# Optimization experiments

Hardware: AMD Instinct MI355X
Metric: run time of the kernel (lower is better)

## Reference

```python
import jax, jax.numpy as jnp
import numpy as np

B, SQ, SE, D, H, DFF = 16, 512, 512, 512, 8, 2048
DH = D // H
EPS = 1e-6


def _ln(x, g, b):
    mu = jnp.mean(x, axis=-1, keepdims=True)
    var = jnp.mean((x - mu) ** 2, axis=-1, keepdims=True)
    return (x - mu) * jax.lax.rsqrt(var + EPS) * g + b


def _mha(v, k, q, mask, wq_w, wq_b, wk_w, wk_b, wv_w, wv_b, do_w, do_b):
    b = q.shape[0]
    def split(t):  # [b, s, D] -> [b, H, s, DH]
        return t.reshape(b, -1, H, DH).transpose(0, 2, 1, 3)
    qh = split(q @ wq_w + wq_b)
    kh = split(k @ wk_w + wk_b)
    vh = split(v @ wv_w + wv_b)
    logits = jnp.einsum('bhqd,bhkd->bhqk', qh, kh) / jnp.sqrt(jnp.float32(DH))
    logits = logits + mask * (-1e9)
    attn = jax.nn.softmax(logits, axis=-1)
    out = jnp.einsum('bhqk,bhkd->bhqd', attn, vh)
    out = out.transpose(0, 2, 1, 3).reshape(b, -1, D)
    # output projection has GELU activation (exact erf, keras default)
    out = jax.nn.gelu(out @ do_w + do_b, approximate=False)
    return out, attn


def setup_inputs() -> dict:
    key = jax.random.key(0)
    ks = jax.random.split(key, 32)
    s = 0.02  # weight scale
    inp = {
        'x': jax.random.normal(ks[0], (B, SQ, D), dtype=jnp.float32),
        'enc_fc': jax.random.normal(ks[1], (B, SE, D), dtype=jnp.float32),
        'enc_ff': jax.random.normal(ks[2], (B, SE, D), dtype=jnp.float32),
        # causal look-ahead mask: 1 where attention is disallowed
        'look_ahead_mask': jnp.triu(jnp.ones((SQ, SQ), jnp.float32), k=1)[None, None],
        # random padding mask over encoder positions (1 = masked)
        'padding_mask': (jax.random.uniform(ks[3], (B, 1, 1, SE)) < 0.1).astype(jnp.float32),
    }
    i = 4
    for p in ('m1', 'm2'):
        for w in ('wq', 'wk', 'wv', 'do'):
            inp[f'{p}_{w}_w'] = jax.random.normal(ks[i], (D, D), dtype=jnp.float32) * s; i += 1
            inp[f'{p}_{w}_b'] = jnp.zeros((D,), jnp.float32)
    inp['ffn_w1'] = jax.random.normal(ks[i], (D, DFF), dtype=jnp.float32) * s; i += 1
    inp['ffn_b1'] = jnp.zeros((DFF,), jnp.float32)
    inp['ffn_w2'] = jax.random.normal(ks[i], (DFF, D), dtype=jnp.float32) * s; i += 1
    inp['ffn_b2'] = jnp.zeros((D,), jnp.float32)
    for ln in ('ln1', 'ln2', 'ln3'):
        inp[f'{ln}_g'] = jnp.ones((D,), jnp.float32)
        inp[f'{ln}_b'] = jnp.zeros((D,), jnp.float32)
    return inp


def reference(x, enc_fc, enc_ff, look_ahead_mask, padding_mask,
              m1_wq_w, m1_wq_b, m1_wk_w, m1_wk_b, m1_wv_w, m1_wv_b, m1_do_w, m1_do_b,
              m2_wq_w, m2_wq_b, m2_wk_w, m2_wk_b, m2_wv_w, m2_wv_b, m2_do_w, m2_do_b,
              ffn_w1, ffn_b1, ffn_w2, ffn_b2,
              ln1_g, ln1_b, ln2_g, ln2_b, ln3_g, ln3_b):
    # self-attention (v=k=q=x), causal mask
    attn1, aw1 = _mha(x, x, x, look_ahead_mask,
                      m1_wq_w, m1_wq_b, m1_wk_w, m1_wk_b, m1_wv_w, m1_wv_b, m1_do_w, m1_do_b)
    out1 = _ln(attn1 + x, ln1_g, ln1_b)  # dropout identity in eval
    # cross-attention: v=enc_ff, k=enc_fc, q=out1, padding mask
    attn2, aw2 = _mha(enc_ff, enc_fc, out1, padding_mask,
                      m2_wq_w, m2_wq_b, m2_wk_w, m2_wk_b, m2_wv_w, m2_wv_b, m2_do_w, m2_do_b)
    out2 = _ln(attn2 + out1, ln2_g, ln2_b)
    # FFN: relu dense -> (dropout identity) -> dense
    ff = jax.nn.relu(out2 @ ffn_w1 + ffn_b1) @ ffn_w2 + ffn_b2
    out3 = _ln(ff + out2, ln3_g, ln3_b)
    return out3, aw1, aw2
```

## Files before the change

kernel.cpp:

```cpp
#include <hip/hip_runtime.h>
#include <stdint.h>
#include <math.h>

typedef unsigned short u16;
typedef __attribute__((ext_vector_type(8))) __bf16 bf16x8;
typedef __attribute__((ext_vector_type(4))) float f32x4;

#define NB 16
#define NSQ 512
#define NSE 512
#define ND 512
#define NH 8
#define NDH 64
#define NDFF 2048

__device__ __forceinline__ u16 f2b(float f) {
  uint32_t u = __float_as_uint(f);
  u = (u + 0x7FFFu + ((u >> 16) & 1u)) >> 16;
  return (u16)u;
}
__device__ __forceinline__ float b2f(uint32_t h) {
  return __uint_as_float(h << 16);
}

__device__ __forceinline__ void gl_lds16(const u16* g, u16* l) {
  __builtin_amdgcn_global_load_lds(
      (const __attribute__((address_space(1))) void*)g,
      (__attribute__((address_space(3))) void*)l, 16, 0, 0);
}

template <int NBX>
__device__ __forceinline__ int swz8(int bx) {
  return (bx & 7) * (NBX / 8) + (bx >> 3);
}

struct Prep {
  const float *x, *fc, *ff;
  u16 *xb, *fcb, *ffb;
  const float* w8[8];
  u16* o8[8];
  const float *w1, *w2;
  u16 *w1t, *w2t;
};

__device__ __forceinline__ void tr32(const float* __restrict__ W,
                                     u16* __restrict__ Wt, int K, int N, int bx,
                                     int by, float (*t)[33]) {
  const int tid = threadIdx.x, tx = tid & 31, ty = tid >> 5;
  const int n0 = bx * 32, k0 = by * 32;
#pragma unroll
  for (int i = 0; i < 32; i += 8)
    t[ty + i][tx] = W[(size_t)(k0 + ty + i) * N + n0 + tx];
  __syncthreads();
#pragma unroll
  for (int i = 0; i < 32; i += 8)
    Wt[(size_t)(n0 + ty + i) * K + k0 + tx] = f2b(t[tx][ty + i]);
}

__global__ void k_prep(Prep p) {
  __shared__ float t[32][33];
  const int blk = blockIdx.x;
  if (blk < 6144) {
    const int plane = blk >> 11;
    const float* src = plane == 0 ? p.x : (plane == 1 ? p.fc : p.ff);
    u16* dst = plane == 0 ? p.xb : (plane == 1 ? p.fcb : p.ffb);
    const int i = (blk & 2047) * 256 + threadIdx.x;
    const float4* q = (const float4*)(src + (size_t)i * 8);
    float4 v0 = q[0], v1 = q[1];
    uint4 o;
    o.x = (uint32_t)f2b(v0.x) | ((uint32_t)f2b(v0.y) << 16);
    o.y = (uint32_t)f2b(v0.z) | ((uint32_t)f2b(v0.w) << 16);
    o.z = (uint32_t)f2b(v1.x) | ((uint32_t)f2b(v1.y) << 16);
    o.w = (uint32_t)f2b(v1.z) | ((uint32_t)f2b(v1.w) << 16);
    *(uint4*)(dst + (size_t)i * 8) = o;
  } else if (blk < 8192) {
    const int b2 = blk - 6144, z = b2 >> 8, bi = b2 & 255;
    tr32(p.w8[z], p.o8[z], 512, 512, bi & 15, bi >> 4, t);
  } else if (blk < 9216) {
    const int b2 = blk - 8192;
    tr32(p.w1, p.w1t, 512, 2048, b2 & 63, b2 >> 6, t);
  } else {
    const int b2 = blk - 9216;
    tr32(p.w2, p.w2t, 2048, 512, b2 & 15, b2 >> 4, t);
  }
}

enum { EPI_GELU = 2, EPI_RELU = 3, EPI_NONE = 4 };

template <int BM>
__device__ __forceinline__ void gemm_core(const u16* __restrict__ A,
                                          const u16* __restrict__ Bt, int K,
                                          int brow, int bcol, u16* As, u16* Bs,
                                          f32x4 (&acc)[BM / 32][4]) {
  const int tid = threadIdx.x, lane = tid & 63, wid = tid >> 6;
  const int wr = wid >> 1, wc = wid & 1;
  const int l15 = lane & 15, g4 = lane >> 4;
  const int sc8 = (lane & 7) * 8;
  const int srow = wid * 8 + (lane >> 3);
  const int nt = K >> 6;
  for (int t = 0; t < nt; ++t) {
    const int k0 = t << 6;
    if (t) __syncthreads();
#pragma unroll
    for (int v = 0; v < BM / 32; ++v)
      gl_lds16(A + (size_t)(brow + v * 32 + srow) * K + k0 + sc8,
               As + (v * 32 + wid * 8) * 64);
#pragma unroll
    for (int v = 0; v < 4; ++v)
      gl_lds16(Bt + (size_t)(bcol + v * 32 + srow) * K + k0 + sc8,
               Bs + (v * 32 + wid * 8) * 64);
    __syncthreads();
#pragma unroll
    for (int kk = 0; kk < 2; ++kk) {
      bf16x8 af[BM / 32], bfr[4];
#pragma unroll
      for (int m = 0; m < BM / 32; ++m)
        af[m] = *(const bf16x8*)(As + (wr * (BM / 2) + m * 16 + l15) * 64 +
                                 kk * 32 + g4 * 8);
#pragma unroll
      for (int n = 0; n < 4; ++n)
        bfr[n] = *(const bf16x8*)(Bs + (wc * 64 + n * 16 + l15) * 64 +
                                  kk * 32 + g4 * 8);
#pragma unroll
      for (int m = 0; m < BM / 32; ++m)
#pragma unroll
        for (int n = 0; n < 4; ++n)
          acc[m][n] =
              __builtin_amdgcn_mfma_f32_16x16x32_bf16(af[m], bfr[n], acc[m][n], 0, 0, 0);
    }
  }
}

template <int BM, int NBX, int EPI>
__global__ __launch_bounds__(256, 3) void k_gemm(
    const u16* __restrict__ A, const u16* __restrict__ Bt,
    const float* __restrict__ bias, u16* __restrict__ out, int K, int N) {
  __shared__ u16 As[BM * 64];
  __shared__ u16 Bs[128 * 64];
  f32x4 acc[BM / 32][4] = {};
  const int brow = swz8<NBX>(blockIdx.x) * BM, bcol = blockIdx.y * 128;
  gemm_core<BM>(A, Bt, K, brow, bcol, As, Bs, acc);
  const int lane = threadIdx.x & 63, wid = threadIdx.x >> 6;
  const int wr = wid >> 1, wc = wid & 1, l15 = lane & 15, g4 = lane >> 4;
#pragma unroll
  for (int m = 0; m < BM / 32; ++m) {
    const int r0 = brow + wr * (BM / 2) + m * 16 + g4 * 4;
#pragma unroll
    for (int n = 0; n < 4; ++n) {
      const int col = bcol + wc * 64 + n * 16 + l15;
      const float bv = bias[col];
#pragma unroll
      for (int j = 0; j < 4; ++j) {
        float vv = acc[m][n][j] + bv;
        if (EPI == EPI_GELU) vv = 0.5f * vv * (1.0f + erff(vv * 0.70710678118654752f));
        if (EPI == EPI_RELU) vv = fmaxf(vv, 0.0f);
        out[(size_t)(r0 + j) * N + col] = f2b(vv);
      }
    }
  }
}

struct QKV {
  const u16* A[3];
  const u16* Bt[3];
  const float* bias[3];
  u16* out[3];
};
__global__ __launch_bounds__(256, 3) void k_gemm_qkv(QKV p) {
  const int z = blockIdx.z;
  __shared__ u16 As[128 * 64];
  __shared__ u16 Bs[128 * 64];
  f32x4 acc[4][4] = {};
  const int brow = swz8<64>(blockIdx.x) * 128, bcol = blockIdx.y * 128;
  gemm_core<128>(p.A[z], p.Bt[z], 512, brow, bcol, As, Bs, acc);
  const int lane = threadIdx.x & 63, wid = threadIdx.x >> 6;
  const int wr = wid >> 1, wc = wid & 1, l15 = lane & 15, g4 = lane >> 4;
  const float* bias = p.bias[z];
  u16* out = p.out[z];
#pragma unroll
  for (int m = 0; m < 4; ++m) {
    const int r0 = brow + wr * 64 + m * 16 + g4 * 4;
#pragma unroll
    for (int n = 0; n < 4; ++n) {
      const int col = bcol + wc * 64 + n * 16 + l15;
      const float bv = bias[col];
      const int h = col >> 6, d = col & 63;
#pragma unroll
      for (int j = 0; j < 4; ++j) {
        const int r = r0 + j, b = r >> 9, s = r & 511;
        const float vv = acc[m][n][j] + bv;
        if (z < 2)
          out[((size_t)(b * NH + h) * NSQ + s) * NDH + d] = f2b(vv);
        else
          out[((size_t)(b * NH + h) * NDH + d) * NSE + s] = f2b(vv);
      }
    }
  }
}

template <int CAUSAL>
__global__ __launch_bounds__(512, 4) void k_attn_fused(
    const u16* __restrict__ qh, const u16* __restrict__ kh,
    const u16* __restrict__ vtg, const float* __restrict__ pmask,
    float* __restrict__ aw, u16* __restrict__ ctx) {
  __shared__ u16 Kt[128 * 64];
  __shared__ u16 Vs[64 * 128];
  __shared__ u16 Ps[128 * 128];

  const int bh = blockIdx.y, b = bh >> 3, h = bh & 7;
  const int brow = blockIdx.x * 128;
  const int tid = threadIdx.x, lane = tid & 63, wid = tid >> 6;
  const int l15 = lane & 15, g4 = lane >> 4;
  const u16* Q = qh + (size_t)bh * NSQ * NDH;
  const u16* Kg = kh + (size_t)bh * NSE * NDH;
  const u16* Vg = vtg + (size_t)bh * NDH * NSE;
  float* awp = aw + (size_t)bh * NSQ * NSE;

  const int krow = wid * 8 + (lane >> 3);
  const int ksw = ((lane & 7) ^ (krow & 7)) * 8;
  const int vsw = (l15 ^ ((wid * 4 + g4) & 7)) * 8;

  bf16x8 qf[2];
#pragma unroll
  for (int kk = 0; kk < 2; ++kk)
    qf[kk] = *(const bf16x8*)(Q + (size_t)(brow + wid * 16 + l15) * NDH +
                              kk * 32 + g4 * 8);

  const int ntile = CAUSAL ? blockIdx.x + 1 : 4;

  auto stage_k = [&](int kb) {
#pragma unroll
    for (int v = 0; v < 2; ++v)
      gl_lds16(Kg + (size_t)(kb + v * 64 + krow) * NDH + ksw,
               Kt + (v * 64 + wid * 8) * 64);
  };
  auto stage_v = [&](int kb) {
#pragma unroll
    for (int v = 0; v < 2; ++v) {
      const int d = v * 32 + wid * 4 + g4;
      gl_lds16(Vg + (size_t)d * NSE + kb + vsw, Vs + (v * 32 + wid * 4) * 128);
    }
  };
  auto computeS = [&](int kb, f32x4(&acc)[8]) {
#pragma unroll
    for (int kk = 0; kk < 2; ++kk) {
      bf16x8 kf[8];
#pragma unroll
      for (int n = 0; n < 8; ++n) {
        const int kr = n * 16 + l15;
        kf[n] = *(const bf16x8*)(Kt + kr * 64 + ((kk * 32 + g4 * 8) ^ ((kr & 7) << 3)));
      }
#pragma unroll
      for (int n = 0; n < 8; ++n)
        acc[n] = __builtin_amdgcn_mfma_f32_16x16x32_bf16(qf[kk], kf[n], acc[n], 0, 0, 0);
    }
    if (!CAUSAL) {
      float pm[8];
#pragma unroll
      for (int n = 0; n < 8; ++n)
        pm[n] = pmask[b * NSE + kb + n * 16 + l15] * (-1e9f);
#pragma unroll
      for (int n = 0; n < 8; ++n)
#pragma unroll
        for (int j = 0; j < 4; ++j)
          acc[n][j] = fminf(acc[n][j] * 0.125f, 60.0f) + pm[n];
    } else {
#pragma unroll
      for (int n = 0; n < 8; ++n) {
        const int key = kb + n * 16 + l15;
#pragma unroll
        for (int j = 0; j < 4; ++j) {
          const int qrow = brow + wid * 16 + g4 * 4 + j;
          acc[n][j] = (key > qrow) ? -1e9f : fminf(acc[n][j] * 0.125f, 60.0f);
        }
      }
    }
  };

  float l4[4] = {0.f, 0.f, 0.f, 0.f};
  for (int t = 0; t < ntile; ++t) {
    if (t) __syncthreads();
    stage_k(t * 128);
    __syncthreads();
    f32x4 acc[8] = {};
    computeS(t * 128, acc);
#pragma unroll
    for (int j = 0; j < 4; ++j) {
      float s = 0.f;
#pragma unroll
      for (int n = 0; n < 8; ++n) s += __expf(acc[n][j]);
#pragma unroll
      for (int o = 1; o < 16; o <<= 1) s += __shfl_xor(s, o, 64);
      l4[j] += s;
    }
  }
  float invl[4];
#pragma unroll
  for (int j = 0; j < 4; ++j) invl[j] = 1.0f / l4[j];

  f32x4 apv[4] = {};
  for (int t = ntile - 1; t >= 0; --t) {
    const int kb = t * 128;
    __syncthreads();
    if (t != ntile - 1) stage_k(kb);
    stage_v(kb);
    __syncthreads();
    f32x4 acc[8] = {};
    computeS(kb, acc);
#pragma unroll
    for (int n = 0; n < 8; ++n) {
      const int col = n * 16 + l15;
#pragma unroll
      for (int j = 0; j < 4; ++j) {
        const int rl = wid * 16 + g4 * 4 + j;
        const float p = __expf(acc[n][j]) * invl[j];
        awp[(size_t)(brow + rl) * NSE + kb + col] = p;
        Ps[rl * 128 + (col ^ ((rl & 7) << 3))] = f2b(p);
      }
    }
#pragma unroll
    for (int kk = 0; kk < 4; ++kk) {
      const int qr = wid * 16 + l15;
      bf16x8 pa =
          *(const bf16x8*)(Ps + qr * 128 + ((kk * 32 + g4 * 8) ^ ((qr & 7) << 3)));
      bf16x8 vb[4];
#pragma unroll
      for (int n = 0; n < 4; ++n) {
        const int d = n * 16 + l15;
        vb[n] = *(const bf16x8*)(Vs + d * 128 + ((kk * 32 + g4 * 8) ^ ((d & 7) << 3)));
      }
#pragma unroll
      for (int n = 0; n < 4; ++n)
        apv[n] = __builtin_amdgcn_mfma_f32_16x16x32_bf16(pa, vb[n], apv[n], 0, 0, 0);
    }
  }

  if (CAUSAL) {
    const float4 z4 = make_float4(0.f, 0.f, 0.f, 0.f);
    for (int t = ntile; t < 4; ++t) {
      const int r = tid >> 2, c0 = t * 128 + (tid & 3) * 32;
      float4* p = (float4*)(awp + (size_t)(brow + r) * NSE + c0);
#pragma unroll
      for (int i = 0; i < 8; ++i) p[i] = z4;
    }
  }

#pragma unroll
  for (int n = 0; n < 4; ++n) {
    const int d = n * 16 + l15;
#pragma unroll
    for (int j = 0; j < 4; ++j) {
      const int r = brow + wid * 16 + g4 * 4 + j;
      ctx[((size_t)(b * NSQ + r)) * ND + h * NDH + d] = f2b(apv[n][j]);
    }
  }
}

template <int B_BF16, int OUT_F32>
__global__ __launch_bounds__(256) void k_res_ln(const u16* __restrict__ a,
                                                const void* __restrict__ bsrc,
                                                const float* __restrict__ g,
                                                const float* __restrict__ bet,
                                                void* __restrict__ outp) {
  const int row = blockIdx.x * 4 + (threadIdx.x >> 6);
  const int lane = threadIdx.x & 63;
  const size_t base = (size_t)row * 512 + lane * 8;
  float s[8];
  {
    uint4 av = *(const uint4*)(a + base);
    s[0] = b2f(av.x & 0xffffu); s[1] = b2f(av.x >> 16);
    s[2] = b2f(av.y & 0xffffu); s[3] = b2f(av.y >> 16);
    s[4] = b2f(av.z & 0xffffu); s[5] = b2f(av.z >> 16);
    s[6] = b2f(av.w & 0xffffu); s[7] = b2f(av.w >> 16);
  }
  if (B_BF16) {
    uint4 bv = *(const uint4*)((const u16*)bsrc + base);
    s[0] += b2f(bv.x & 0xffffu); s[1] += b2f(bv.x >> 16);
    s[2] += b2f(bv.y & 0xffffu); s[3] += b2f(bv.y >> 16);
    s[4] += b2f(bv.z & 0xffffu); s[5] += b2f(bv.z >> 16);
    s[6] += b2f(bv.w & 0xffffu); s[7] += b2f(bv.w >> 16);
  } else {
    const float* bp = (const float*)bsrc + base;
    float4 b0 = *(const float4*)bp, b1 = *(const float4*)(bp + 4);
    s[0] += b0.x; s[1] += b0.y; s[2] += b0.z; s[3] += b0.w;
    s[4] += b1.x; s[5] += b1.y; s[6] += b1.z; s[7] += b1.w;
  }
  float sum = 0.f;
#pragma unroll
  for (int i = 0; i < 8; ++i) sum += s[i];
#pragma unroll
  for (int o = 1; o < 64; o <<= 1) sum += __shfl_xor(sum, o, 64);
  const float mu = sum * (1.0f / 512.0f);
  float vs = 0.f;
#pragma unroll
  for (int i = 0; i < 8; ++i) {
    const float d = s[i] - mu;
    vs += d * d;
  }
#pragma unroll
  for (int o = 1; o < 64; o <<= 1) vs += __shfl_xor(vs, o, 64);
  const float rs = rsqrtf(vs * (1.0f / 512.0f) + 1e-6f);
  float y[8];
#pragma unroll
  for (int i = 0; i < 8; ++i) {
    const int c = lane * 8 + i;
    y[i] = (s[i] - mu) * rs * g[c] + bet[c];
  }
  if (OUT_F32) {
    float* op = (float*)outp + base;
    *(float4*)op = make_float4(y[0], y[1], y[2], y[3]);
    *(float4*)(op + 4) = make_float4(y[4], y[5], y[6], y[7]);
  } else {
    uint4 o;
    o.x = (uint32_t)f2b(y[0]) | ((uint32_t)f2b(y[1]) << 16);
    o.y = (uint32_t)f2b(y[2]) | ((uint32_t)f2b(y[3]) << 16);
    o.z = (uint32_t)f2b(y[4]) | ((uint32_t)f2b(y[5]) << 16);
    o.w = (uint32_t)f2b(y[6]) | ((uint32_t)f2b(y[7]) << 16);
    *(uint4*)((u16*)outp + base) = o;
  }
}

extern "C" void kernel_launch(void* const* d_in, const int* in_sizes, int n_in,
                              void* d_out, int out_size, void* d_ws, size_t ws_size,
                              hipStream_t stream) {
  (void)in_sizes; (void)n_in; (void)out_size; (void)ws_size;
  const float* x = (const float*)d_in[0];
  const float* enc_fc = (const float*)d_in[1];
  const float* enc_ff = (const float*)d_in[2];
  const float* pmask = (const float*)d_in[4];
  const float* w_m1[4] = {(const float*)d_in[5], (const float*)d_in[7],
                          (const float*)d_in[9], (const float*)d_in[11]};
  const float* b_m1[4] = {(const float*)d_in[6], (const float*)d_in[8],
                          (const float*)d_in[10], (const float*)d_in[12]};
  const float* w_m2[4] = {(const float*)d_in[13], (const float*)d_in[15],
                          (const float*)d_in[17], (const float*)d_in[19]};
  const float* b_m2[4] = {(const float*)d_in[14], (const float*)d_in[16],
                          (const float*)d_in[18], (const float*)d_in[20]};
  const float* ffn_w1 = (const float*)d_in[21];
  const float* ffn_b1 = (const float*)d_in[22];
  const float* ffn_w2 = (const float*)d_in[23];
  const float* ffn_b2 = (const float*)d_in[24];
  const float* ln_g[3] = {(const float*)d_in[25], (const float*)d_in[27],
                          (const float*)d_in[29]};
  const float* ln_b[3] = {(const float*)d_in[26], (const float*)d_in[28],
                          (const float*)d_in[30]};

  char* ws = (char*)d_ws;
  const size_t SZB = (size_t)8192 * 512 * 2;
  u16* xb = (u16*)(ws + 0 * SZB);
  u16* fcb = (u16*)(ws + 1 * SZB);
  u16* ffb = (u16*)(ws + 2 * SZB);
  u16* qh = (u16*)(ws + 3 * SZB);
  u16* kh = (u16*)(ws + 4 * SZB);
  u16* vt = (u16*)(ws + 5 * SZB);
  u16* ctx = (u16*)(ws + 6 * SZB);
  u16* ao = (u16*)(ws + 7 * SZB);
  u16* out1 = (u16*)(ws + 8 * SZB);
  u16* out2 = (u16*)(ws + 9 * SZB);
  u16* ffv = (u16*)(ws + 10 * SZB);
  u16* ff1 = (u16*)(ws + 11 * SZB);
  u16* wts = (u16*)(ws + 11 * SZB + (size_t)8192 * 2048 * 2);
  u16 *wt_m1[4], *wt_m2[4];
  for (int i = 0; i < 4; ++i) {
    wt_m1[i] = wts + (size_t)i * 262144;
    wt_m2[i] = wts + (size_t)(4 + i) * 262144;
  }
  u16* w1t = wts + (size_t)8 * 262144;
  u16* w2t = w1t + (size_t)2048 * 512;

  float* out3 = (float*)d_out;
  float* aw1 = out3 + (size_t)NB * NSQ * ND;
  float* aw2 = aw1 + (size_t)NB * NH * NSQ * NSQ;

  Prep pr;
  pr.x = x; pr.fc = enc_fc; pr.ff = enc_ff;
  pr.xb = xb; pr.fcb = fcb; pr.ffb = ffb;
  for (int i = 0; i < 4; ++i) {
    pr.w8[i] = w_m1[i]; pr.o8[i] = wt_m1[i];
    pr.w8[4 + i] = w_m2[i]; pr.o8[4 + i] = wt_m2[i];
  }
  pr.w1 = ffn_w1; pr.w1t = w1t;
  pr.w2 = ffn_w2; pr.w2t = w2t;
  k_prep<<<10240, 256, 0, stream>>>(pr);

  const dim3 gattn(4, 128);
  QKV q1 = {{xb, xb, xb},
            {wt_m1[0], wt_m1[1], wt_m1[2]},
            {b_m1[0], b_m1[1], b_m1[2]},
            {qh, kh, vt}};
  k_gemm_qkv<<<dim3(64, 4, 3), 256, 0, stream>>>(q1);
  k_attn_fused<1><<<gattn, 512, 0, stream>>>(qh, kh, vt, nullptr, aw1, ctx);
  k_gemm<64, 128, EPI_GELU><<<dim3(128, 4), 256, 0, stream>>>(ctx, wt_m1[3], b_m1[3], ao, 512, 512);
  k_res_ln<0, 0><<<2048, 256, 0, stream>>>(ao, x, ln_g[0], ln_b[0], out1);
  QKV q2 = {{out1, fcb, ffb},
            {wt_m2[0], wt_m2[1], wt_m2[2]},
            {b_m2[0], b_m2[1], b_m2[2]},
            {qh, kh, vt}};
  k_gemm_qkv<<<dim3(64, 4, 3), 256, 0, stream>>>(q2);
  k_attn_fused<0><<<gattn, 512, 0, stream>>>(qh, kh, vt, pmask, aw2, ctx);
  k_gemm<64, 128, EPI_GELU><<<dim3(128, 4), 256, 0, stream>>>(ctx, wt_m2[3], b_m2[3], ao, 512, 512);
  k_res_ln<1, 0><<<2048, 256, 0, stream>>>(ao, out1, ln_g[1], ln_b[1], out2);
  k_gemm<128, 64, EPI_RELU><<<dim3(64, 16), 256, 0, stream>>>(out2, w1t, ffn_b1, ff1, 512, 2048);
  k_gemm<64, 128, EPI_NONE><<<dim3(128, 4), 256, 0, stream>>>(ff1, w2t, ffn_b2, ffv, 2048, 512);
  k_res_ln<1, 1><<<2048, 256, 0, stream>>>(ffv, out2, ln_g[2], ln_b[2], (void*)d_out);
}
```

Baseline: 328.4 us.

## Hoist cross-attention K/V projections into first QKV launch and reuse last score tile

The cross-attention K and V projections depend only on encoder inputs, so they move into the first QKV GEMM launch (grid z=5). This fills the grid better and leaves the second launch with only the Q projection. They write into the out2/ffv scratch buffers, which are not used until later. The attention kernel keeps the exponentiated scores of the last tile from pass one, skipping one K restage and score recompute. Attention-weight output is now written as coalesced float4 stores read back from the bf16 Ps tile, which rounds aw1/aw2 to bf16 precision.

Measured after the change: 333.8 us. Within noise of the previous version (+1.7%).

```diff
diff --git a/kernel.cpp b/kernel.cpp
--- a/kernel.cpp
+++ b/kernel.cpp
@@ -161,10 +161,11 @@
 }
 
 struct QKV {
-  const u16* A[3];
-  const u16* Bt[3];
-  const float* bias[3];
-  u16* out[3];
+  const u16* A[5];
+  const u16* Bt[5];
+  const float* bias[5];
+  u16* out[5];
+  int vout[5];
 };
 __global__ __launch_bounds__(256, 3) void k_gemm_qkv(QKV p) {
   const int z = blockIdx.z;
@@ -177,6 +178,7 @@
   const int wr = wid >> 1, wc = wid & 1, l15 = lane & 15, g4 = lane >> 4;
   const float* bias = p.bias[z];
   u16* out = p.out[z];
+  const int vl = p.vout[z];
 #pragma unroll
   for (int m = 0; m < 4; ++m) {
     const int r0 = brow + wr * 64 + m * 16 + g4 * 4;
@@ -189,7 +191,7 @@
       for (int j = 0; j < 4; ++j) {
         const int r = r0 + j, b = r >> 9, s = r & 511;
         const float vv = acc[m][n][j] + bv;
-        if (z < 2)
+        if (vl == 0)
           out[((size_t)(b * NH + h) * NSQ + s) * NDH + d] = f2b(vv);
         else
           out[((size_t)(b * NH + h) * NDH + d) * NSE + s] = f2b(vv);
@@ -278,6 +280,7 @@
   };
 
   float l4[4] = {0.f, 0.f, 0.f, 0.f};
+  f32x4 pcar[8];
   for (int t = 0; t < ntile; ++t) {
     if (t) __syncthreads();
     stage_k(t * 128);
@@ -285,38 +288,47 @@
     f32x4 acc[8] = {};
     computeS(t * 128, acc);
 #pragma unroll
+    for (int n = 0; n < 8; ++n)
+#pragma unroll
+      for (int j = 0; j < 4; ++j) acc[n][j] = __expf(acc[n][j]);
+#pragma unroll
     for (int j = 0; j < 4; ++j) {
       float s = 0.f;
 #pragma unroll
-      for (int n = 0; n < 8; ++n) s += __expf(acc[n][j]);
+      for (int n = 0; n < 8; ++n) s += acc[n][j];
 #pragma unroll
       for (int o = 1; o < 16; o <<= 1) s += __shfl_xor(s, o, 64);
       l4[j] += s;
     }
+    if (t == ntile - 1)
+#pragma unroll
+      for (int n = 0; n < 8; ++n) pcar[n] = acc[n];
   }
   float invl[4];
 #pragma unroll
   for (int j = 0; j < 4; ++j) invl[j] = 1.0f / l4[j];
 
   f32x4 apv[4] = {};
-  for (int t = ntile - 1; t >= 0; --t) {
-    const int kb = t * 128;
-    __syncthreads();
-    if (t != ntile - 1) stage_k(kb);
-    stage_v(kb);
-    __syncthreads();
-    f32x4 acc[8] = {};
-    computeS(kb, acc);
+  auto emitTile = [&](f32x4(&pex)[8], int kb) {
 #pragma unroll
     for (int n = 0; n < 8; ++n) {
       const int col = n * 16 + l15;
 #pragma unroll
       for (int j = 0; j < 4; ++j) {
         const int rl = wid * 16 + g4 * 4 + j;
-        const float p = __expf(acc[n][j]) * invl[j];
-        awp[(size_t)(brow + rl) * NSE + kb + col] = p;
-        Ps[rl * 128 + (col ^ ((rl & 7) << 3))] = f2b(p);
+        Ps[rl * 128 + (col ^ ((rl & 7) << 3))] = f2b(pex[n][j] * invl[j]);
       }
+    }
+#pragma unroll
+    for (int i = 0; i < 4; ++i) {
+      const int rl = wid * 16 + i * 4 + (lane >> 4);
+      const int cb = l15 * 8;
+      uint4 pk = *(const uint4*)(Ps + rl * 128 + (cb ^ ((rl & 7) << 3)));
+      float* dst = awp + (size_t)(brow + rl) * NSE + kb + cb;
+      *(float4*)dst = make_float4(b2f(pk.x & 0xffffu), b2f(pk.x >> 16),
+                                  b2f(pk.y & 0xffffu), b2f(pk.y >> 16));
+      *(float4*)(dst + 4) = make_float4(b2f(pk.z & 0xffffu), b2f(pk.z >> 16),
+                                        b2f(pk.w & 0xffffu), b2f(pk.w >> 16));
     }
 #pragma unroll
     for (int kk = 0; kk < 4; ++kk) {
@@ -333,6 +345,27 @@
       for (int n = 0; n < 4; ++n)
         apv[n] = __builtin_amdgcn_mfma_f32_16x16x32_bf16(pa, vb[n], apv[n], 0, 0, 0);
     }
+  };
+
+  {
+    const int kb = (ntile - 1) * 128;
+    stage_v(kb);
+    __syncthreads();
+    emitTile(pcar, kb);
+  }
+  for (int t = ntile - 2; t >= 0; --t) {
+    const int kb = t * 128;
+    __syncthreads();
+    stage_k(kb);
+    stage_v(kb);
+    __syncthreads();
+    f32x4 acc[8] = {};
+    computeS(kb, acc);
+#pragma unroll
+    for (int n = 0; n < 8; ++n)
+#pragma unroll
+      for (int j = 0; j < 4; ++j) acc[n][j] = __expf(acc[n][j]);
+    emitTile(acc, kb);
   }
 
   if (CAUSAL) {
@@ -468,6 +501,9 @@
   u16* w1t = wts + (size_t)8 * 262144;
   u16* w2t = w1t + (size_t)2048 * 512;
 
+  u16* kh2 = out2;
+  u16* vt2 = ffv;
+
   float* out3 = (float*)d_out;
   float* aw1 = out3 + (size_t)NB * NSQ * ND;
   float* aw2 = aw1 + (size_t)NB * NH * NSQ * NSQ;
@@ -484,20 +520,22 @@
   k_prep<<<10240, 256, 0, stream>>>(pr);
 
   const dim3 gattn(4, 128);
-  QKV q1 = {{xb, xb, xb},
-            {wt_m1[0], wt_m1[1], wt_m1[2]},
-            {b_m1[0], b_m1[1], b_m1[2]},
-            {qh, kh, vt}};
-  k_gemm_qkv<<<dim3(64, 4, 3), 256, 0, stream>>>(q1);
+  QKV q1 = {{xb, xb, xb, fcb, ffb},
+            {wt_m1[0], wt_m1[1], wt_m1[2], wt_m2[1], wt_m2[2]},
+            {b_m1[0], b_m1[1], b_m1[2], b_m2[1], b_m2[2]},
+            {qh, kh, vt, kh2, vt2},
+            {0, 0, 1, 0, 1}};
+  k_gemm_qkv<<<dim3(64, 4, 5), 256, 0, stream>>>(q1);
   k_attn_fused<1><<<gattn, 512, 0, stream>>>(qh, kh, vt, nullptr, aw1, ctx);
   k_gemm<64, 128, EPI_GELU><<<dim3(128, 4), 256, 0, stream>>>(ctx, wt_m1[3], b_m1[3], ao, 512, 512);
   k_res_ln<0, 0><<<2048, 256, 0, stream>>>(ao, x, ln_g[0], ln_b[0], out1);
-  QKV q2 = {{out1, fcb, ffb},
-            {wt_m2[0], wt_m2[1], wt_m2[2]},
-            {b_m2[0], b_m2[1], b_m2[2]},
-            {qh, kh, vt}};
-  k_gemm_qkv<<<dim3(64, 4, 3), 256, 0, stream>>>(q2);
-  k_attn_fused<0><<<gattn, 512, 0, stream>>>(qh, kh, vt, pmask, aw2, ctx);
+  QKV q2 = {{out1, nullptr, nullptr, nullptr, nullptr},
+            {wt_m2[0], nullptr, nullptr, nullptr, nullptr},
+            {b_m2[0], nullptr, nullptr, nullptr, nullptr},
+            {qh, nullptr, nullptr, nullptr, nullptr},
+            {0, 0, 0, 0, 0}};
+  k_gemm_qkv<<<dim3(64, 4, 1), 256, 0, stream>>>(q2);
+  k_attn_fused<0><<<gattn, 512, 0, stream>>>(qh, kh2, vt2, pmask, aw2, ctx);
   k_gemm<64, 128, EPI_GELU><<<dim3(128, 4), 256, 0, stream>>>(ctx, wt_m2[3], b_m2[3], ao, 512, 512);
   k_res_ln<1, 0><<<2048, 256, 0, stream>>>(ao, out1, ln_g[1], ln_b[1], out2);
   k_gemm<128, 64, EPI_RELU><<<dim3(64, 16), 256, 0, stream>>>(out2, w1t, ffn_b1, ff1, 512, 2048);
```

## Double-buffer GEMM LDS tiles and hoist cross-attention K/V projections into first QKV launch

Applied to the files above, without the earlier changes.

The GEMM core now uses double-buffered LDS so the next K-tile's global-to-LDS load is issued while MFMAs run on the current tile. Every GEMM is fixed to a 64x128 tile, and the occupancy hint is raised to 4 blocks per CU. The encoder-side K/V projections for cross-attention depend only on inputs, so they now run in the first QKV launch as extra z-slices, leaving the second launch to compute only Q. Their results are stored in the out2/ffv buffers, which are free until later; this saves one full pass worth of launch and tail overhead but ties correctness to buffer lifetimes.

Result: no change. 334.8 us (+2.0%).

```diff
diff --git a/kernel.cpp b/kernel.cpp
--- a/kernel.cpp
+++ b/kernel.cpp
@@ -87,64 +87,70 @@
 
 enum { EPI_GELU = 2, EPI_RELU = 3, EPI_NONE = 4 };
 
-template <int BM>
-__device__ __forceinline__ void gemm_core(const u16* __restrict__ A,
-                                          const u16* __restrict__ Bt, int K,
-                                          int brow, int bcol, u16* As, u16* Bs,
-                                          f32x4 (&acc)[BM / 32][4]) {
+__device__ __forceinline__ void gemm_core2(const u16* __restrict__ A,
+                                           const u16* __restrict__ Bt, int K,
+                                           int brow, int bcol, u16* As, u16* Bs,
+                                           f32x4 (&acc)[2][4]) {
   const int tid = threadIdx.x, lane = tid & 63, wid = tid >> 6;
   const int wr = wid >> 1, wc = wid & 1;
   const int l15 = lane & 15, g4 = lane >> 4;
   const int sc8 = (lane & 7) * 8;
   const int srow = wid * 8 + (lane >> 3);
   const int nt = K >> 6;
-  for (int t = 0; t < nt; ++t) {
+  const int ASZ = 64 * 64, BSZ = 128 * 64;
+  auto stage = [&](int t, int buf) {
     const int k0 = t << 6;
-    if (t) __syncthreads();
-#pragma unroll
-    for (int v = 0; v < BM / 32; ++v)
+#pragma unroll
+    for (int v = 0; v < 2; ++v)
       gl_lds16(A + (size_t)(brow + v * 32 + srow) * K + k0 + sc8,
-               As + (v * 32 + wid * 8) * 64);
+               As + buf * ASZ + (v * 32 + wid * 8) * 64);
 #pragma unroll
     for (int v = 0; v < 4; ++v)
       gl_lds16(Bt + (size_t)(bcol + v * 32 + srow) * K + k0 + sc8,
-               Bs + (v * 32 + wid * 8) * 64);
-    __syncthreads();
+               Bs + buf * BSZ + (v * 32 + wid * 8) * 64);
+  };
+  stage(0, 0);
+  __syncthreads();
+  int cur = 0;
+  for (int t = 0; t < nt; ++t) {
+    if (t + 1 < nt) stage(t + 1, cur ^ 1);
+    const u16* as = As + cur * ASZ;
+    const u16* bs = Bs + cur * BSZ;
 #pragma unroll
     for (int kk = 0; kk < 2; ++kk) {
-      bf16x8 af[BM / 32], bfr[4];
-#pragma unroll
-      for (int m = 0; m < BM / 32; ++m)
-        af[m] = *(const bf16x8*)(As + (wr * (BM / 2) + m * 16 + l15) * 64 +
-                                 kk * 32 + g4 * 8);
+      bf16x8 af[2], bfr[4];
+#pragma unroll
+      for (int m = 0; m < 2; ++m)
+        af[m] = *(const bf16x8*)(as + (wr * 32 + m * 16 + l15) * 64 + kk * 32 + g4 * 8);
 #pragma unroll
       for (int n = 0; n < 4; ++n)
-        bfr[n] = *(const bf16x8*)(Bs + (wc * 64 + n * 16 + l15) * 64 +
-                                  kk * 32 + g4 * 8);
-#pragma unroll
-      for (int m = 0; m < BM / 32; ++m)
+        bfr[n] = *(const bf16x8*)(bs + (wc * 64 + n * 16 + l15) * 64 + kk * 32 + g4 * 8);
+#pragma unroll
+      for (int m = 0; m < 2; ++m)
 #pragma unroll
         for (int n = 0; n < 4; ++n)
           acc[m][n] =
               __builtin_amdgcn_mfma_f32_16x16x32_bf16(af[m], bfr[n], acc[m][n], 0, 0, 0);
     }
-  }
-}
-
-template <int BM, int NBX, int EPI>
-__global__ __launch_bounds__(256, 3) void k_gemm(
+    __syncthreads();
+    cur ^= 1;
+  }
+}
+
+template <int NBX, int EPI>
+__global__ __launch_bounds__(256, 4) void k_gemm(
     const u16* __restrict__ A, const u16* __restrict__ Bt,
     const float* __restrict__ bias, u16* __restrict__ out, int K, int N) {
-  __shared__ u16 As[BM * 64];
-  __shared__ u16 Bs[128 * 64];
-  f32x4 acc[BM / 32][4] = {};
-  const int brow = swz8<NBX>(blockIdx.x) * BM, bcol = blockIdx.y * 128;
-  gemm_core<BM>(A, Bt, K, brow, bcol, As, Bs, acc);
+  __shared__ u16 As[2 * 64 * 64];
+  __shared__ u16 Bs[2 * 128 * 64];
+  f32x4 acc[2][4] = {};
+  const int brow = swz8<NBX>(blockIdx.x) * 64, bcol = blockIdx.y * 128;
+  gemm_core2(A, Bt, K, brow, bcol, As, Bs, acc);
   const int lane = threadIdx.x & 63, wid = threadIdx.x >> 6;
   const int wr = wid >> 1, wc = wid & 1, l15 = lane & 15, g4 = lane >> 4;
 #pragma unroll
-  for (int m = 0; m < BM / 32; ++m) {
-    const int r0 = brow + wr * (BM / 2) + m * 16 + g4 * 4;
+  for (int m = 0; m < 2; ++m) {
+    const int r0 = brow + wr * 32 + m * 16 + g4 * 4;
 #pragma unroll
     for (int n = 0; n < 4; ++n) {
       const int col = bcol + wc * 64 + n * 16 + l15;
@@ -161,25 +167,27 @@
 }
 
 struct QKV {
-  const u16* A[3];
-  const u16* Bt[3];
-  const float* bias[3];
-  u16* out[3];
+  const u16* A[5];
+  const u16* Bt[5];
+  const float* bias[5];
+  u16* out[5];
+  int vout[5];
 };
-__global__ __launch_bounds__(256, 3) void k_gemm_qkv(QKV p) {
+__global__ __launch_bounds__(256, 4) void k_gemm_qkv(QKV p) {
   const int z = blockIdx.z;
-  __shared__ u16 As[128 * 64];
-  __shared__ u16 Bs[128 * 64];
-  f32x4 acc[4][4] = {};
-  const int brow = swz8<64>(blockIdx.x) * 128, bcol = blockIdx.y * 128;
-  gemm_core<128>(p.A[z], p.Bt[z], 512, brow, bcol, As, Bs, acc);
+  __shared__ u16 As[2 * 64 * 64];
+  __shared__ u16 Bs[2 * 128 * 64];
+  f32x4 acc[2][4] = {};
+  const int brow = swz8<128>(blockIdx.x) * 64, bcol = blockIdx.y * 128;
+  gemm_core2(p.A[z], p.Bt[z], 512, brow, bcol, As, Bs, acc);
   const int lane = threadIdx.x & 63, wid = threadIdx.x >> 6;
   const int wr = wid >> 1, wc = wid & 1, l15 = lane & 15, g4 = lane >> 4;
   const float* bias = p.bias[z];
   u16* out = p.out[z];
-#pragma unroll
-  for (int m = 0; m < 4; ++m) {
-    const int r0 = brow + wr * 64 + m * 16 + g4 * 4;
+  const int vl = p.vout[z];
+#pragma unroll
+  for (int m = 0; m < 2; ++m) {
+    const int r0 = brow + wr * 32 + m * 16 + g4 * 4;
 #pragma unroll
     for (int n = 0; n < 4; ++n) {
       const int col = bcol + wc * 64 + n * 16 + l15;
@@ -189,7 +197,7 @@
       for (int j = 0; j < 4; ++j) {
         const int r = r0 + j, b = r >> 9, s = r & 511;
         const float vv = acc[m][n][j] + bv;
-        if (z < 2)
+        if (vl == 0)
           out[((size_t)(b * NH + h) * NSQ + s) * NDH + d] = f2b(vv);
         else
           out[((size_t)(b * NH + h) * NDH + d) * NSE + s] = f2b(vv);
@@ -468,6 +476,9 @@
   u16* w1t = wts + (size_t)8 * 262144;
   u16* w2t = w1t + (size_t)2048 * 512;
 
+  u16* kh2 = out2;
+  u16* vt2 = ffv;
+
   float* out3 = (float*)d_out;
   float* aw1 = out3 + (size_t)NB * NSQ * ND;
   float* aw2 = aw1 + (size_t)NB * NH * NSQ * NSQ;
@@ -484,23 +495,25 @@
   k_prep<<<10240, 256, 0, stream>>>(pr);
 
   const dim3 gattn(4, 128);
-  QKV q1 = {{xb, xb, xb},
-            {wt_m1[0], wt_m1[1], wt_m1[2]},
-            {b_m1[0], b_m1[1], b_m1[2]},
-            {qh, kh, vt}};
-  k_gemm_qkv<<<dim3(64, 4, 3), 256, 0, stream>>>(q1);
+  QKV q1 = {{xb, xb, xb, fcb, ffb},
+            {wt_m1[0], wt_m1[1], wt_m1[2], wt_m2[1], wt_m2[2]},
+            {b_m1[0], b_m1[1], b_m1[2], b_m2[1], b_m2[2]},
+            {qh, kh, vt, kh2, vt2},
+            {0, 0, 1, 0, 1}};
+  k_gemm_qkv<<<dim3(128, 4, 5), 256, 0, stream>>>(q1);
   k_attn_fused<1><<<gattn, 512, 0, stream>>>(qh, kh, vt, nullptr, aw1, ctx);
-  k_gemm<64, 128, EPI_GELU><<<dim3(128, 4), 256, 0, stream>>>(ctx, wt_m1[3], b_m1[3], ao, 512, 512);
+  k_gemm<128, EPI_GELU><<<dim3(128, 4), 256, 0, stream>>>(ctx, wt_m1[3], b_m1[3], ao, 512, 512);
   k_res_ln<0, 0><<<2048, 256, 0, stream>>>(ao, x, ln_g[0], ln_b[0], out1);
-  QKV q2 = {{out1, fcb, ffb},
-            {wt_m2[0], wt_m2[1], wt_m2[2]},
-            {b_m2[0], b_m2[1], b_m2[2]},
-            {qh, kh, vt}};
-  k_gemm_qkv<<<dim3(64, 4, 3), 256, 0, stream>>>(q2);
-  k_attn_fused<0><<<gattn, 512, 0, stream>>>(qh, kh, vt, pmask, aw2, ctx);
-  k_gemm<64, 128, EPI_GELU><<<dim3(128, 4), 256, 0, stream>>>(ctx, wt_m2[3], b_m2[3], ao, 512, 512);
+  QKV q2 = {{out1, nullptr, nullptr, nullptr, nullptr},
+            {wt_m2[0], nullptr, nullptr, nullptr, nullptr},
+            {b_m2[0], nullptr, nullptr, nullptr, nullptr},
+            {qh, nullptr, nullptr, nullptr, nullptr},
+            {0, 0, 0, 0, 0}};
+  k_gemm_qkv<<<dim3(128, 4, 1), 256, 0, stream>>>(q2);
+  k_attn_fused<0><<<gattn, 512, 0, stream>>>(qh, kh2, vt2, pmask, aw2, ctx);
+  k_gemm<128, EPI_GELU><<<dim3(128, 4), 256, 0, stream>>>(ctx, wt_m2[3], b_m2[3], ao, 512, 512);
   k_res_ln<1, 0><<<2048, 256, 0, stream>>>(ao, out1, ln_g[1], ln_b[1], out2);
-  k_gemm<128, 64, EPI_RELU><<<dim3(64, 16), 256, 0, stream>>>(out2, w1t, ffn_b1, ff1, 512, 2048);
-  k_gemm<64, 128, EPI_NONE><<<dim3(128, 4), 256, 0, stream>>>(ff1, w2t, ffn_b2, ffv, 2048, 512);
+  k_gemm<128, EPI_RELU><<<dim3(128, 16), 256, 0, stream>>>(out2, w1t, ffn_b1, ff1, 512, 2048);
+  k_gemm<128, EPI_NONE><<<dim3(128, 4), 256, 0, stream>>>(ff1, w2t, ffn_b2, ffv, 2048, 512);
   k_res_ln<1, 1><<<2048, 256, 0, stream>>>(ffv, out2, ln_g[2], ln_b[2], (void*)d_out);
 }
```

## Double-buffer K tiles in attention, balance causal block order, use nontemporal stores

Applied to the files above, without the earlier changes.

The attention kernel now double-buffers the K tile in shared memory, so the next tile is prefetched while the current one is computed, and one barrier per iteration is removed. The 1D grid is remapped so causal query blocks are ordered heavy/light in a balanced way: the first half of the grid takes row blocks 0,1 and the second half takes 3,2. Attention-weight stores and the zero fill now use nontemporal stores to avoid polluting the cache. This adds 16KB of shared memory per block, which may lower occupancy.

Result: slower. 352.8 us (+7.4%).

```diff
diff --git a/kernel.cpp b/kernel.cpp
--- a/kernel.cpp
+++ b/kernel.cpp
@@ -203,12 +203,17 @@
     const u16* __restrict__ qh, const u16* __restrict__ kh,
     const u16* __restrict__ vtg, const float* __restrict__ pmask,
     float* __restrict__ aw, u16* __restrict__ ctx) {
-  __shared__ u16 Kt[128 * 64];
+  __shared__ u16 Kt[2][128 * 64];
   __shared__ u16 Vs[64 * 128];
   __shared__ u16 Ps[128 * 128];
 
-  const int bh = blockIdx.y, b = bh >> 3, h = bh & 7;
-  const int brow = blockIdx.x * 128;
+  const int jb = blockIdx.x;
+  const int lo = jb & 255;
+  const int bh = lo & 127;
+  const int sel = lo >> 7;
+  const int bx = (jb >> 8) == 0 ? sel : 3 - sel;
+  const int b = bh >> 3, h = bh & 7;
+  const int brow = bx * 128;
   const int tid = threadIdx.x, lane = tid & 63, wid = tid >> 6;
   const int l15 = lane & 15, g4 = lane >> 4;
   const u16* Q = qh + (size_t)bh * NSQ * NDH;
@@ -226,13 +231,13 @@
     qf[kk] = *(const bf16x8*)(Q + (size_t)(brow + wid * 16 + l15) * NDH +
                               kk * 32 + g4 * 8);
 
-  const int ntile = CAUSAL ? blockIdx.x + 1 : 4;
-
-  auto stage_k = [&](int kb) {
+  const int ntile = CAUSAL ? bx + 1 : 4;
+
+  auto stage_k = [&](int kb, int buf) {
 #pragma unroll
     for (int v = 0; v < 2; ++v)
       gl_lds16(Kg + (size_t)(kb + v * 64 + krow) * NDH + ksw,
-               Kt + (v * 64 + wid * 8) * 64);
+               Kt[buf] + (v * 64 + wid * 8) * 64);
   };
   auto stage_v = [&](int kb) {
 #pragma unroll
@@ -241,14 +246,15 @@
       gl_lds16(Vg + (size_t)d * NSE + kb + vsw, Vs + (v * 32 + wid * 4) * 128);
     }
   };
-  auto computeS = [&](int kb, f32x4(&acc)[8]) {
+  auto computeS = [&](int kb, int buf, f32x4(&acc)[8]) {
+    const u16* kt = Kt[buf];
 #pragma unroll
     for (int kk = 0; kk < 2; ++kk) {
       bf16x8 kf[8];
 #pragma unroll
       for (int n = 0; n < 8; ++n) {
         const int kr = n * 16 + l15;
-        kf[n] = *(const bf16x8*)(Kt + kr * 64 + ((kk * 32 + g4 * 8) ^ ((kr & 7) << 3)));
+        kf[n] = *(const bf16x8*)(kt + kr * 64 + ((kk * 32 + g4 * 8) ^ ((kr & 7) << 3)));
       }
 #pragma unroll
       for (int n = 0; n < 8; ++n)
@@ -278,12 +284,13 @@
   };
 
   float l4[4] = {0.f, 0.f, 0.f, 0.f};
+  stage_k(0, 0);
+  __syncthreads();
   for (int t = 0; t < ntile; ++t) {
-    if (t) __syncthreads();
-    stage_k(t * 128);
-    __syncthreads();
+    const int cur = t & 1;
+    if (t + 1 < ntile) stage_k((t + 1) * 128, cur ^ 1);
     f32x4 acc[8] = {};
-    computeS(t * 128, acc);
+    computeS(t * 128, cur, acc);
 #pragma unroll
     for (int j = 0; j < 4; ++j) {
       float s = 0.f;
@@ -293,6 +300,7 @@
       for (int o = 1; o < 16; o <<= 1) s += __shfl_xor(s, o, 64);
       l4[j] += s;
     }
+    __syncthreads();
   }
   float invl[4];
 #pragma unroll
@@ -301,12 +309,12 @@
   f32x4 apv[4] = {};
   for (int t = ntile - 1; t >= 0; --t) {
     const int kb = t * 128;
+    const int cur = t & 1;
+    if (t > 0) stage_k((t - 1) * 128, cur ^ 1);
+    stage_v(kb);
+    f32x4 acc[8] = {};
+    computeS(kb, cur, acc);
     __syncthreads();
-    if (t != ntile - 1) stage_k(kb);
-    stage_v(kb);
-    __syncthreads();
-    f32x4 acc[8] = {};
-    computeS(kb, acc);
 #pragma unroll
     for (int n = 0; n < 8; ++n) {
       const int col = n * 16 + l15;
@@ -314,7 +322,7 @@
       for (int j = 0; j < 4; ++j) {
         const int rl = wid * 16 + g4 * 4 + j;
         const float p = __expf(acc[n][j]) * invl[j];
-        awp[(size_t)(brow + rl) * NSE + kb + col] = p;
+        __builtin_nontemporal_store(p, awp + (size_t)(brow + rl) * NSE + kb + col);
         Ps[rl * 128 + (col ^ ((rl & 7) << 3))] = f2b(p);
       }
     }
@@ -333,15 +341,16 @@
       for (int n = 0; n < 4; ++n)
         apv[n] = __builtin_amdgcn_mfma_f32_16x16x32_bf16(pa, vb[n], apv[n], 0, 0, 0);
     }
+    __syncthreads();
   }
 
   if (CAUSAL) {
-    const float4 z4 = make_float4(0.f, 0.f, 0.f, 0.f);
+    const f32x4 z4 = {0.f, 0.f, 0.f, 0.f};
     for (int t = ntile; t < 4; ++t) {
       const int r = tid >> 2, c0 = t * 128 + (tid & 3) * 32;
-      float4* p = (float4*)(awp + (size_t)(brow + r) * NSE + c0);
-#pragma unroll
-      for (int i = 0; i < 8; ++i) p[i] = z4;
+      f32x4* p = (f32x4*)(awp + (size_t)(brow + r) * NSE + c0);
+#pragma unroll
+      for (int i = 0; i < 8; ++i) __builtin_nontemporal_store(z4, p + i);
     }
   }
 
@@ -483,13 +492,12 @@
   pr.w2 = ffn_w2; pr.w2t = w2t;
   k_prep<<<10240, 256, 0, stream>>>(pr);
 
-  const dim3 gattn(4, 128);
   QKV q1 = {{xb, xb, xb},
             {wt_m1[0], wt_m1[1], wt_m1[2]},
             {b_m1[0], b_m1[1], b_m1[2]},
             {qh, kh, vt}};
   k_gemm_qkv<<<dim3(64, 4, 3), 256, 0, stream>>>(q1);
-  k_attn_fused<1><<<gattn, 512, 0, stream>>>(qh, kh, vt, nullptr, aw1, ctx);
+  k_attn_fused<1><<<512, 512, 0, stream>>>(qh, kh, vt, nullptr, aw1, ctx);
   k_gemm<64, 128, EPI_GELU><<<dim3(128, 4), 256, 0, stream>>>(ctx, wt_m1[3], b_m1[3], ao, 512, 512);
   k_res_ln<0, 0><<<2048, 256, 0, stream>>>(ao, x, ln_g[0], ln_b[0], out1);
   QKV q2 = {{out1, fcb, ffb},
@@ -497,7 +505,7 @@
             {b_m2[0], b_m2[1], b_m2[2]},
             {qh, kh, vt}};
   k_gemm_qkv<<<dim3(64, 4, 3), 256, 0, stream>>>(q2);
-  k_attn_fused<0><<<gattn, 512, 0, stream>>>(qh, kh, vt, pmask, aw2, ctx);
+  k_attn_fused<0><<<512, 512, 0, stream>>>(qh, kh, vt, pmask, aw2, ctx);
   k_gemm<64, 128, EPI_GELU><<<dim3(128, 4), 256, 0, stream>>>(ctx, wt_m2[3], b_m2[3], ao, 512, 512);
   k_res_ln<1, 0><<<2048, 256, 0, stream>>>(ao, out1, ln_g[1], ln_b[1], out2);
   k_gemm<128, 64, EPI_RELU><<<dim3(64, 16), 256, 0, stream>>>(out2, w1t, ffn_b1, ff1, 512, 2048);
```
